# Kernel optimization log

Hardware: AMD Instinct MI355X
Metric: run time of the kernel (lower is better)

## Reference

```python
import jax, jax.numpy as jnp
import numpy as np

N, E, G = 50000, 800000, 16
NODE, HID, OUT, HEADS = 128, 64, 128, 3
NEG_SLOPE = 0.2

def setup_inputs() -> dict:
    key = jax.random.key(0)
    ks = jax.random.split(key, 12)
    h = jax.random.normal(ks[0], (N, NODE), jnp.float32)
    z = jax.random.normal(ks[1], (G, OUT), jnp.float32)
    src = jax.random.randint(ks[2], (E,), 0, N, jnp.int32)
    dst = jax.random.randint(ks[3], (E,), 0, N, jnp.int32)
    graph_id = jnp.sort(jax.random.randint(ks[4], (N,), 0, G, jnp.int32))
    s = 0.1
    fc_w = jax.random.normal(ks[5], (HEADS * HID, NODE), jnp.float32) * s
    attn_l = jax.random.normal(ks[6], (HEADS, HID), jnp.float32) * s
    attn_r = jax.random.normal(ks[7], (HEADS, HID), jnp.float32) * s
    bias = jnp.zeros((HEADS * HID,), jnp.float32)
    lin1_w = jax.random.normal(ks[8], (HID, OUT), jnp.float32) * s
    lin1_b = jnp.zeros((HID,), jnp.float32)
    lin2_w = jax.random.normal(ks[9], (1, 2 * HID), jnp.float32) * s
    lin2_b = jnp.zeros((1,), jnp.float32)
    return dict(h=h, z=z, src=src, dst=dst, graph_id=graph_id, fc_w=fc_w,
                attn_l=attn_l, attn_r=attn_r, bias=bias,
                lin1_w=lin1_w, lin1_b=lin1_b, lin2_w=lin2_w, lin2_b=lin2_b)

def reference(h, z, src, dst, graph_id, fc_w, attn_l, attn_r, bias,
              lin1_w, lin1_b, lin2_w, lin2_b):
    n = h.shape[0]
    # GATConv: projection -> [N, H, D]
    feat = (h @ fc_w.T).reshape(n, HEADS, HID)
    el = jnp.sum(feat * attn_l, axis=-1)  # [N, H]
    er = jnp.sum(feat * attn_r, axis=-1)  # [N, H]
    e = jax.nn.leaky_relu(el[src] + er[dst], NEG_SLOPE)  # [E, H]
    # edge softmax per destination node
    m = jax.ops.segment_max(e, dst, num_segments=n)
    e = jnp.exp(e - m[dst])
    s = jax.ops.segment_sum(e, dst, num_segments=n)
    alpha = e / s[dst]
    # scatter-weighted aggregation
    msg = alpha[:, :, None] * feat[src]  # [E, H, D]
    rst = jax.ops.segment_sum(msg, dst, num_segments=n)  # [N, H, D]
    rst = rst + bias.reshape(HEADS, HID)
    h_d = jnp.mean(rst, axis=1)  # [N, D] (mean over heads)
    # dgl.mean_nodes: per-graph mean pooling
    counts = jax.ops.segment_sum(jnp.ones((n,), h_d.dtype), graph_id, num_segments=G)
    pooled = jax.ops.segment_sum(h_d, graph_id, num_segments=G) / jnp.maximum(counts, 1.0)[:, None]
    z1 = z @ lin1_w.T + lin1_b  # [G, HID]
    cat = jnp.concatenate([pooled, z1], axis=1)  # [G, 2*HID]
    score = jax.nn.sigmoid(cat @ lin2_w.T + lin2_b)  # [G, 1]
    return score
```

## Files before the change

### kernel.cpp

```cpp
#include <hip/hip_runtime.h>
#include <math.h>

#define N_NODES 50000
#define N_EDGES 800000
#define N_GRAPHS 16
#define NODE_F 128
#define HID 64
#define OUT_F 128
#define HEADS 3
#define NEG 0.2f
#define FEAT (HEADS*HID)

typedef float f32x4 __attribute__((ext_vector_type(4)));
typedef float f32x2 __attribute__((ext_vector_type(2)));
typedef short bf16x8 __attribute__((ext_vector_type(8)));

#if defined(__has_builtin)
#if __has_builtin(__builtin_amdgcn_cvt_pk_f32_fp8) && __has_builtin(__builtin_amdgcn_cvt_pk_fp8_f32)
#define USE_FP8 1
#endif
#endif
#ifndef USE_FP8
#define USE_FP8 0
#endif

#if USE_FP8
#define FB 1
#else
#define FB 2
#endif
#define ROWB (FEAT * FB)

#define NBKT ((N_NODES + 63) / 64)
#define H1B 400
#define EPB (N_EDGES / H1B)
#define LROW2 208

__device__ __forceinline__ ushort f2bf(float x) {
  union { float f; unsigned u; } v; v.f = x;
  unsigned r = v.u + 0x7fff + ((v.u >> 16) & 1);
  return (ushort)(r >> 16);
}
__device__ __forceinline__ float bf2f(ushort x) {
  union { unsigned u; float f; } v; v.u = ((unsigned)x) << 16;
  return v.f;
}

__device__ __forceinline__ void feat_store(unsigned char* base, int n, int hh, int dd, float v) {
  size_t off = (size_t)n * ROWB + (hh * HID + dd) * FB;
#if USE_FP8
  base[off] = (unsigned char)(__builtin_amdgcn_cvt_pk_fp8_f32(v, 0.f, 0, false) & 0xff);
#else
  *(ushort*)(base + off) = f2bf(v);
#endif
}

#define ZERO_INTS (N_GRAPHS * HID + N_GRAPHS)
#define ZERO_U4 (ZERO_INTS / 4)
#define ZB ((ZERO_U4 + 255) / 256)
__global__ void kprep(const float* __restrict__ fc_w, ushort* __restrict__ fcb,
                      uint4* __restrict__ zbase) {
  if (blockIdx.x >= 24) {
    int i = (blockIdx.x - 24) * 256 + threadIdx.x;
    if (i < ZERO_U4) zbase[i] = make_uint4(0, 0, 0, 0);
    return;
  }
  int i = blockIdx.x * 256 + threadIdx.x;
  int col = i >> 5;
  int kb = (i & 31) * 4;
  float4 v = *(const float4*)(fc_w + (size_t)col * NODE_F + kb);
  int t = col >> 4, m = col & 15;
  int kk = kb >> 5, kq = (kb >> 3) & 3, j = kb & 7;
  size_t idx0 = ((((size_t)t * 4 + kk) * 4 + kq) * 16 + m) * 8 + j;
  ushort4 o; o.x = f2bf(v.x); o.y = f2bf(v.y); o.z = f2bf(v.z); o.w = f2bf(v.w);
  *(ushort4*)(fcb + idx0) = o;
}

#define GB0 ((N_NODES + 63) / 64)
__global__ __launch_bounds__(256) void k01_fused(
    const float* __restrict__ h, const ushort* __restrict__ fcb,
    const float* __restrict__ attn_l, const float* __restrict__ attn_r,
    const int* __restrict__ dst,
    unsigned char* __restrict__ feat, float* __restrict__ el, float* __restrict__ er,
    int* __restrict__ cnt_g)
{
  __shared__ ushort A[64][136];
  const int tid = threadIdx.x;

  if (blockIdx.x < H1B) {
    int* cnt = (int*)&A[0][0];
    const int blk = blockIdx.x;
    for (int i = tid; i < NBKT; i += 256) cnt[i] = 0;
    __syncthreads();
    const int e0 = blk * EPB;
    for (int i = tid; i < EPB; i += 256)
      atomicAdd(&cnt[dst[e0 + i] >> 6], 1);
    __syncthreads();
    for (int i = tid; i < NBKT; i += 256) cnt_g[(size_t)blk * NBKT + i] = cnt[i];
    return;
  }

  const int n0 = (blockIdx.x - H1B) * 64;
  for (int i = tid; i < 64 * 32; i += 256) {
    int r = i >> 5, c4 = i & 31;
    if (n0 + r < N_NODES) {
      float4 v = *(const float4*)(h + (size_t)(n0 + r) * NODE_F + c4 * 4);
      unsigned lo = f2bf(v.x) | ((unsigned)f2bf(v.y) << 16);
      unsigned hi = f2bf(v.z) | ((unsigned)f2bf(v.w) << 16);
      *(uint2*)&A[r][c4 * 4] = make_uint2(lo, hi);
    }
  }
  __syncthreads();

  const int lane = tid & 63, wv = tid >> 6;
  const int m = lane & 15, kq = lane >> 4;

  f32x4 acc[12];
#pragma unroll
  for (int t = 0; t < 12; t++) acc[t] = (f32x4){0.f, 0.f, 0.f, 0.f};

#pragma unroll
  for (int kk = 0; kk < 4; kk++) {
    bf16x8 af = *(const bf16x8*)&A[wv * 16 + m][kk * 32 + kq * 8];
#pragma unroll
    for (int t = 0; t < 12; t++) {
      const bf16x8 bf = *(const bf16x8*)(fcb + ((((size_t)t * 4 + kk) * 4 + kq) * 16 + m) * 8);
      acc[t] = __builtin_amdgcn_mfma_f32_16x16x32_bf16(af, bf, acc[t], 0, 0, 0);
    }
  }

  const int rbase = n0 + wv * 16 + kq * 4;

#if USE_FP8
  __syncthreads();
  unsigned char* lf = (unsigned char*)&A[0][0];
  const int rloc = wv * 16 + kq * 4;
#pragma unroll
  for (int t = 0; t < 12; t++) {
    const int hh = t >> 2;
    const int dd = (t & 3) * 16 + m;
    const int boff = hh * HID + dd;
#pragma unroll
    for (int reg = 0; reg < 4; reg++) {
      unsigned char q = (unsigned char)(__builtin_amdgcn_cvt_pk_fp8_f32(acc[t][reg], 0.f, 0, false) & 0xff);
      lf[(rloc + reg) * LROW2 + boff] = q;
    }
  }
#else
#pragma unroll
  for (int t = 0; t < 12; t++) {
    const int hh = t >> 2;
    const int dd = (t & 3) * 16 + m;
#pragma unroll
    for (int reg = 0; reg < 4; reg++) {
      int n = rbase + reg;
      if (n < N_NODES) feat_store(feat, n, hh, dd, acc[t][reg]);
    }
  }
#endif

#pragma unroll
  for (int hh = 0; hh < HEADS; hh++) {
    float elv[4] = {0.f, 0.f, 0.f, 0.f};
    float erv[4] = {0.f, 0.f, 0.f, 0.f};
#pragma unroll
    for (int tt = 0; tt < 4; tt++) {
      int t = hh * 4 + tt;
      float al = attn_l[hh * HID + tt * 16 + m];
      float ar = attn_r[hh * HID + tt * 16 + m];
#pragma unroll
      for (int reg = 0; reg < 4; reg++) {
        elv[reg] = fmaf(acc[t][reg], al, elv[reg]);
        erv[reg] = fmaf(acc[t][reg], ar, erv[reg]);
      }
    }
#pragma unroll
    for (int reg = 0; reg < 4; reg++) {
#pragma unroll
      for (int off = 1; off < 16; off <<= 1) {
        elv[reg] += __shfl_xor(elv[reg], off, 64);
        erv[reg] += __shfl_xor(erv[reg], off, 64);
      }
      int n = rbase + reg;
      if (m == 0 && n < N_NODES) {
        el[(size_t)n * 4 + hh] = elv[reg];
        er[(size_t)n * 4 + hh] = erv[reg];
      }
    }
  }

#if USE_FP8
  __syncthreads();
  for (int i = tid; i < 64 * (ROWB / 16); i += 256) {
    int r = i / (ROWB / 16), c = (i % (ROWB / 16)) * 16;
    int n = n0 + r;
    if (n < N_NODES)
      *(uint4*)(feat + (size_t)n * ROWB + c) = *(const uint4*)(lf + r * LROW2 + c);
  }
#endif
}

#define H2A_K 7
__global__ __launch_bounds__(64) void kh2a_scan(
    const int* __restrict__ cnt_g, int* __restrict__ base_bm, int* __restrict__ btot)
{
  const int b = blockIdx.x;
  const int lane = threadIdx.x;
  int v[H2A_K];
  int lt = 0;
#pragma unroll
  for (int j = 0; j < H2A_K; j++) {
    int g = lane * H2A_K + j;
    v[j] = (g < H1B) ? cnt_g[(size_t)g * NBKT + b] : 0;
    lt += v[j];
  }
  int s = lt;
#pragma unroll
  for (int off = 1; off < 64; off <<= 1) {
    int t = __shfl_up(s, off, 64);
    if (lane >= off) s += t;
  }
  int excl = s - lt;
#pragma unroll
  for (int j = 0; j < H2A_K; j++) {
    int g = lane * H2A_K + j;
    if (g < H1B) base_bm[(size_t)b * H1B + g] = excl;
    excl += v[j];
  }
  if (lane == 63) btot[b] = s;
}

__global__ __launch_bounds__(256) void kh3_scatter(
    const int* __restrict__ src, const int* __restrict__ dst,
    const int* __restrict__ btot, const int* __restrict__ base_bm,
    int2* __restrict__ pairs)
{
  __shared__ int cur[NBKT];
  __shared__ int wsum[4];
  const int tid = threadIdx.x, blk = blockIdx.x;
  const int lane = tid & 63, wv = tid >> 6;
  int v[4]; int lt = 0;
#pragma unroll
  for (int j = 0; j < 4; j++) {
    int g = tid * 4 + j;
    v[j] = (g < NBKT) ? btot[g] : 0;
    lt += v[j];
  }
  int s = lt;
#pragma unroll
  for (int off = 1; off < 64; off <<= 1) {
    int t = __shfl_up(s, off, 64);
    if (lane >= off) s += t;
  }
  if (lane == 63) wsum[wv] = s;
  __syncthreads();
  int woff = 0;
#pragma unroll
  for (int w = 0; w < 4; w++) woff += (w < wv) ? wsum[w] : 0;
  int excl = s - lt + woff;
#pragma unroll
  for (int j = 0; j < 4; j++) {
    int g = tid * 4 + j;
    if (g < NBKT) cur[g] = excl + base_bm[(size_t)g * H1B + blk];
    excl += v[j];
  }
  __syncthreads();
  const int e0 = blk * EPB;
  for (int i = tid; i < EPB; i += 256) {
    int e = e0 + i;
    int d = dst[e], sv = src[e];
    int slot = atomicAdd(&cur[d >> 6], 1);
    pairs[slot] = make_int2(sv, d);
  }
}

__global__ __launch_bounds__(256) void kh4_nodesort(
    const int2* __restrict__ pairs, const int* __restrict__ btot,
    int* __restrict__ src_s, int* __restrict__ offs)
{
  __shared__ int nodecnt[64];
  __shared__ int cur[64];
  __shared__ int red_[4];
  __shared__ int lo_s, hi_s;
  const int b = blockIdx.x, tid = threadIdx.x;
  const int lane = tid & 63, wv = tid >> 6;
  int partial = 0;
  for (int i = tid; i < b; i += 256) partial += btot[i];
#pragma unroll
  for (int off = 32; off; off >>= 1) partial += __shfl_xor(partial, off, 64);
  if (lane == 0) red_[wv] = partial;
  if (tid < 64) nodecnt[tid] = 0;
  __syncthreads();
  if (tid == 0) {
    int l = red_[0] + red_[1] + red_[2] + red_[3];
    lo_s = l; hi_s = l + btot[b];
  }
  __syncthreads();
  const int lo = lo_s, hi = hi_s;
  for (int i = lo + tid; i < hi; i += 256)
    atomicAdd(&nodecnt[pairs[i].y & 63], 1);
  __syncthreads();
  if (tid < 64) {
    int v = nodecnt[tid];
    int s = v;
#pragma unroll
    for (int off = 1; off < 64; off <<= 1) {
      int t = __shfl_up(s, off, 64);
      if (tid >= off) s += t;
    }
    int excl = s - v;
    cur[tid] = lo + excl;
    int n = b * 64 + tid;
    if (n < N_NODES) offs[n] = lo + excl;
    if (b == NBKT - 1 && tid == 0) offs[N_NODES] = N_EDGES;
  }
  __syncthreads();
  for (int i = lo + tid; i < hi; i += 256) {
    int2 pr = pairs[i];
    int slot = atomicAdd(&cur[pr.y & 63], 1);
    src_s[slot] = pr.x;
  }
}

__global__ __launch_bounds__(256) void k4_agg(
    const int* __restrict__ offs, const int* __restrict__ src_s,
    const float* __restrict__ el4, const float* __restrict__ er4,
    const unsigned char* __restrict__ feat, const float* __restrict__ bias,
    float* __restrict__ h_d)
{
  __shared__ float4 rec[4][64];
  const int wv = threadIdx.x >> 6, lane = threadIdx.x & 63;
  const int n = blockIdx.x * 4 + wv;
  const int lo = offs[n], hi = offs[n + 1];
  const int half = lane >> 5;
  const int d = lane & 31;
  const char* fb = (const char*)feat;
  const float4 ern = ((const float4*)er4)[n];

  float a0x = 0.f, a0y = 0.f, a1x = 0.f, a1y = 0.f, a2x = 0.f, a2y = 0.f;
  float s0 = 0.f, s1 = 0.f, s2 = 0.f;

  for (int base = lo; base < hi; base += 64) {
    const int cnt = min(64, hi - base);
    if (lane < cnt) {
      int sidx = src_s[base + lane];
      float4 elv = ((const float4*)el4)[sidx];
      float e0 = elv.x + ern.x; e0 = e0 > 0.f ? e0 : NEG * e0;
      float e1 = elv.y + ern.y; e1 = e1 > 0.f ? e1 : NEG * e1;
      float e2 = elv.z + ern.z; e2 = e2 > 0.f ? e2 : NEG * e2;
      float4 c;
      c.x = __expf(e0); c.y = __expf(e1); c.z = __expf(e2);
      c.w = __int_as_float(sidx * ROWB);
      rec[wv][lane] = c;
      s0 += c.x; s1 += c.y; s2 += c.z;
    }
#define K4_BODY(J) do { \
      float4 c = rec[wv][J]; \
      f32x2 f0, f1, f2; \
      if (USE_FP8) { \
        const char* rp = fb + __float_as_int(c.w) + 2 * d; \
        ushort u0 = *(const ushort*)(rp); \
        ushort u1 = *(const ushort*)(rp + HID); \
        ushort u2 = *(const ushort*)(rp + 2 * HID); \
        f0 = __builtin_amdgcn_cvt_pk_f32_fp8(u0, false); \
        f1 = __builtin_amdgcn_cvt_pk_f32_fp8(u1, false); \
        f2 = __builtin_amdgcn_cvt_pk_f32_fp8(u2, false); \
      } else { \
        const char* rp = fb + __float_as_int(c.w) + 4 * d; \
        unsigned q0 = *(const unsigned*)(rp); \
        unsigned q1 = *(const unsigned*)(rp + 2 * HID); \
        unsigned q2 = *(const unsigned*)(rp + 4 * HID); \
        f0.x = bf2f((ushort)(q0 & 0xffff)); f0.y = bf2f((ushort)(q0 >> 16)); \
        f1.x = bf2f((ushort)(q1 & 0xffff)); f1.y = bf2f((ushort)(q1 >> 16)); \
        f2.x = bf2f((ushort)(q2 & 0xffff)); f2.y = bf2f((ushort)(q2 >> 16)); \
      } \
      a0x = fmaf(c.x, f0.x, a0x); a0y = fmaf(c.x, f0.y, a0y); \
      a1x = fmaf(c.y, f1.x, a1x); a1y = fmaf(c.y, f1.y, a1y); \
      a2x = fmaf(c.z, f2.x, a2x); a2y = fmaf(c.z, f2.y, a2y); \
    } while (0)
    int j = half;
    for (; j + 2 < cnt; j += 4) { K4_BODY(j); K4_BODY(j + 2); }
    if (j < cnt) K4_BODY(j);
#undef K4_BODY
  }
  a0x += __shfl_xor(a0x, 32, 64); a0y += __shfl_xor(a0y, 32, 64);
  a1x += __shfl_xor(a1x, 32, 64); a1y += __shfl_xor(a1y, 32, 64);
  a2x += __shfl_xor(a2x, 32, 64); a2y += __shfl_xor(a2y, 32, 64);
#pragma unroll
  for (int off = 32; off; off >>= 1) {
    s0 += __shfl_xor(s0, off, 64);
    s1 += __shfl_xor(s1, off, 64);
    s2 += __shfl_xor(s2, off, 64);
  }
  const float i0 = s0 > 0.f ? 1.f / s0 : 0.f;
  const float i1 = s1 > 0.f ? 1.f / s1 : 0.f;
  const float i2 = s2 > 0.f ? 1.f / s2 : 0.f;
  if (half == 0) {
    float2 b0 = *(const float2*)(bias + 2 * d);
    float2 b1 = *(const float2*)(bias + HID + 2 * d);
    float2 b2 = *(const float2*)(bias + 2 * HID + 2 * d);
    float2 o;
    o.x = (fmaf(a0x, i0, b0.x) + fmaf(a1x, i1, b1.x) + fmaf(a2x, i2, b2.x)) * (1.f / 3.f);
    o.y = (fmaf(a0y, i0, b0.y) + fmaf(a1y, i1, b1.y) + fmaf(a2y, i2, b2.y)) * (1.f / 3.f);
    *(float2*)(h_d + (size_t)n * HID + 2 * d) = o;
  }
}

#define K5_NPB 128
#define K5_NB ((N_NODES + K5_NPB - 1) / K5_NPB)
#define NSEG (K5_NB * 2)
__global__ __launch_bounds__(256) void k5a_partial(
    const int* __restrict__ graph_id, const float* __restrict__ h_d,
    float* __restrict__ pooled_res, int* __restrict__ gcnt_res,
    float* __restrict__ part, int* __restrict__ pg, int* __restrict__ pc)
{
  const int wv = threadIdx.x >> 6, lane = threadIdx.x & 63;
  const int b = blockIdx.x;
  const int n0 = b * K5_NPB;
  const int n1 = min(n0 + K5_NPB, N_NODES);
  const int g_lo = graph_id[n0], g_hi = graph_id[n1 - 1];

  if (g_hi > g_lo + 1) {
    float acc = 0.f; int cur_g = -1; int cnt = 0;
    for (int i = n0 + wv; i < n1; i += 4) {
      int g = graph_id[i];
      if (g != cur_g) {
        if (cur_g >= 0) {
          atomicAdd(&pooled_res[cur_g * HID + lane], acc);
          if (lane == 0) atomicAdd(&gcnt_res[cur_g], cnt);
        }
        acc = 0.f; cnt = 0; cur_g = g;
      }
      acc += h_d[(size_t)i * HID + lane];
      cnt++;
    }
    if (cur_g >= 0) {
      atomicAdd(&pooled_res[cur_g * HID + lane], acc);
      if (lane == 0) atomicAdd(&gcnt_res[cur_g], cnt);
    }
    if (threadIdx.x < 2) pg[b * 2 + threadIdx.x] = -1;
    return;
  }

  float acc_lo = 0.f, acc_hi = 0.f;
  int c_lo = 0, c_hi = 0;
  for (int i = n0 + wv; i < n1; i += 4) {
    int g = graph_id[i];
    float v = h_d[(size_t)i * HID + lane];
    bool hi = (g != g_lo);
    acc_hi += hi ? v : 0.f;
    acc_lo += hi ? 0.f : v;
    c_hi += hi ? 1 : 0;
    c_lo += hi ? 0 : 1;
  }
  __shared__ float ls[2][4][64];
  __shared__ int lc[2][4];
  ls[0][wv][lane] = acc_lo;
  ls[1][wv][lane] = acc_hi;
  if (lane == 0) { lc[0][wv] = c_lo; lc[1][wv] = c_hi; }
  __syncthreads();
  if (wv < 2) {
    float s = ls[wv][0][lane] + ls[wv][1][lane] + ls[wv][2][lane] + ls[wv][3][lane];
    part[((size_t)b * 2 + wv) * HID + lane] = s;
    if (lane == 0) {
      int cnt = lc[wv][0] + lc[wv][1] + lc[wv][2] + lc[wv][3];
      int gg = (wv == 0) ? g_lo : g_hi;
      if (wv == 1 && (g_hi == g_lo || cnt == 0)) gg = -1;
      pg[b * 2 + wv] = gg;
      pc[b * 2 + wv] = cnt;
    }
  }
}

__global__ __launch_bounds__(256) void k6_final(
    const float* __restrict__ part, const int* __restrict__ pg, const int* __restrict__ pc,
    const float* __restrict__ pooled_res, const int* __restrict__ gcnt_res,
    const float* __restrict__ z,
    const float* __restrict__ lin1_w, const float* __restrict__ lin1_b,
    const float* __restrict__ lin2_w, const float* __restrict__ lin2_b,
    float* __restrict__ out)
{
  const int g = blockIdx.x;
  const int tid = threadIdx.x, wv = tid >> 6, lane = tid & 63;
  __shared__ int spg[NSEG], spc[NSEG];
  __shared__ float red[4][HID];
  __shared__ int rc[4];
  __shared__ float cat[2 * HID];

  for (int i = tid; i < NSEG; i += 256) { spg[i] = pg[i]; spc[i] = pc[i]; }
  __syncthreads();

  float acc = 0.f; int cnt = 0;
  for (int s = wv; s < NSEG; s += 4) {
    if (spg[s] == g) {
      acc += part[(size_t)s * HID + lane];
      cnt += spc[s];
    }
  }
  red[wv][lane] = acc;
  if (lane == 0) rc[wv] = cnt;
  __syncthreads();

  if (wv == 0) {
    float s = red[0][lane] + red[1][lane] + red[2][lane] + red[3][lane]
            + pooled_res[g * HID + lane];
    int c = rc[0] + rc[1] + rc[2] + rc[3] + gcnt_res[g];
    cat[lane] = s / (float)(c > 0 ? c : 1);
  }
  if (wv == 1) {
    float s = lin1_b[lane];
    const float* zr = z + g * OUT_F;
    const float* wr = lin1_w + lane * OUT_F;
    for (int k = 0; k < OUT_F; k += 4) {
      float4 zv = *(const float4*)(zr + k);
      float4 wv4 = *(const float4*)(wr + k);
      s = fmaf(zv.x, wv4.x, fmaf(zv.y, wv4.y, fmaf(zv.z, wv4.z, fmaf(zv.w, wv4.w, s))));
    }
    cat[HID + lane] = s;
  }
  __syncthreads();
  if (wv == 0) {
    float s = cat[lane] * lin2_w[lane] + cat[HID + lane] * lin2_w[HID + lane];
#pragma unroll
    for (int off = 32; off; off >>= 1) s += __shfl_xor(s, off, 64);
    if (lane == 0) out[g] = 1.f / (1.f + __expf(-(s + lin2_b[0])));
  }
}

extern "C" void kernel_launch(void* const* d_in, const int* in_sizes, int n_in,
                              void* d_out, int out_size, void* d_ws, size_t ws_size,
                              hipStream_t stream) {
  (void)in_sizes; (void)n_in; (void)out_size; (void)ws_size;
  const float* h      = (const float*)d_in[0];
  const float* z      = (const float*)d_in[1];
  const int*   src    = (const int*)d_in[2];
  const int*   dst    = (const int*)d_in[3];
  const int*   gid    = (const int*)d_in[4];
  const float* fc_w   = (const float*)d_in[5];
  const float* attn_l = (const float*)d_in[6];
  const float* attn_r = (const float*)d_in[7];
  const float* bias   = (const float*)d_in[8];
  const float* lin1_w = (const float*)d_in[9];
  const float* lin1_b = (const float*)d_in[10];
  const float* lin2_w = (const float*)d_in[11];
  const float* lin2_b = (const float*)d_in[12];
  float* out = (float*)d_out;

  int2* pairs       = (int2*)d_ws;
  unsigned char* feat = (unsigned char*)(pairs + N_EDGES);
  float* h_d        = (float*)(feat + (size_t)N_NODES * ROWB);
  float* el         = h_d + (size_t)N_NODES * HID;
  float* er         = el + (size_t)N_NODES * 4;
  float* part       = er + (size_t)N_NODES * 4;
  int* pg           = (int*)(part + (size_t)NSEG * HID);
  int* pc           = pg + NSEG;
  ushort* fcb       = (ushort*)(pc + NSEG);
  float* pooled_res = (float*)(fcb + 192 * NODE_F);
  int* gcnt_res     = (int*)(pooled_res + N_GRAPHS * HID);
  int* offs         = gcnt_res + N_GRAPHS;
  int* src_s        = offs + (N_NODES + 1);
  int* cnt_g        = src_s + N_EDGES;
  int* base_bm      = cnt_g + (size_t)H1B * NBKT;
  int* btot         = base_bm + (size_t)NBKT * H1B;

  kprep<<<24 + ZB, 256, 0, stream>>>(fc_w, fcb, (uint4*)pooled_res);
  k01_fused<<<H1B + GB0, 256, 0, stream>>>(h, fcb, attn_l, attn_r, dst,
                                           feat, el, er, cnt_g);
  kh2a_scan<<<NBKT, 64, 0, stream>>>(cnt_g, base_bm, btot);
  kh3_scatter<<<H1B, 256, 0, stream>>>(src, dst, btot, base_bm, pairs);
  kh4_nodesort<<<NBKT, 256, 0, stream>>>(pairs, btot, src_s, offs);
  k4_agg<<<N_NODES / 4, 256, 0, stream>>>(offs, src_s, el, er, feat, bias, h_d);
  k5a_partial<<<K5_NB, 256, 0, stream>>>(gid, h_d, pooled_res, gcnt_res, part, pg, pc);
  k6_final<<<N_GRAPHS, 256, 0, stream>>>(part, pg, pc, pooled_res, gcnt_res,
                                         z, lin1_w, lin1_b, lin2_w, lin2_b, out);
}
```

Baseline: 202.4 us.

## Merge sort and pooling kernel chains into cooperative kernels with grid sync

Replaces the three-kernel edge bucketing sequence (scan, scatter, node sort) with one cooperative kernel separated by grid-wide syncs. The pooling partial and final scoring kernels are merged the same way. This removes kernel launch gaps and inter-kernel drain between small dependent stages. In exchange it adds grid barrier costs and requires all blocks to be co-resident, with the scatter phase assuming H1B is no larger than NBKT.

```diff
diff --git a/kernel.cpp b/kernel.cpp
--- a/kernel.cpp
+++ b/kernel.cpp
@@ -1,5 +1,8 @@
 #include <hip/hip_runtime.h>
+#include <hip/hip_cooperative_groups.h>
 #include <math.h>
+
+namespace cg = cooperative_groups;
 
 #define N_NODES 50000
 #define N_EDGES 800000
@@ -201,124 +204,124 @@
 }
 
 #define H2A_K 7
-__global__ __launch_bounds__(64) void kh2a_scan(
-    const int* __restrict__ cnt_g, int* __restrict__ base_bm, int* __restrict__ btot)
+__global__ __launch_bounds__(256) void ksort_coop(
+    const int* __restrict__ src, const int* __restrict__ dst,
+    const int* __restrict__ cnt_g, int* __restrict__ base_bm, int* __restrict__ btot,
+    int2* __restrict__ pairs, int* __restrict__ src_s, int* __restrict__ offs)
 {
-  const int b = blockIdx.x;
-  const int lane = threadIdx.x;
-  int v[H2A_K];
-  int lt = 0;
-#pragma unroll
-  for (int j = 0; j < H2A_K; j++) {
-    int g = lane * H2A_K + j;
-    v[j] = (g < H1B) ? cnt_g[(size_t)g * NBKT + b] : 0;
-    lt += v[j];
-  }
-  int s = lt;
-#pragma unroll
-  for (int off = 1; off < 64; off <<= 1) {
-    int t = __shfl_up(s, off, 64);
-    if (lane >= off) s += t;
-  }
-  int excl = s - lt;
-#pragma unroll
-  for (int j = 0; j < H2A_K; j++) {
-    int g = lane * H2A_K + j;
-    if (g < H1B) base_bm[(size_t)b * H1B + g] = excl;
-    excl += v[j];
-  }
-  if (lane == 63) btot[b] = s;
-}
-
-__global__ __launch_bounds__(256) void kh3_scatter(
-    const int* __restrict__ src, const int* __restrict__ dst,
-    const int* __restrict__ btot, const int* __restrict__ base_bm,
-    int2* __restrict__ pairs)
-{
+  cg::grid_group grid = cg::this_grid();
   __shared__ int cur[NBKT];
   __shared__ int wsum[4];
-  const int tid = threadIdx.x, blk = blockIdx.x;
-  const int lane = tid & 63, wv = tid >> 6;
-  int v[4]; int lt = 0;
-#pragma unroll
-  for (int j = 0; j < 4; j++) {
-    int g = tid * 4 + j;
-    v[j] = (g < NBKT) ? btot[g] : 0;
-    lt += v[j];
-  }
-  int s = lt;
-#pragma unroll
-  for (int off = 1; off < 64; off <<= 1) {
-    int t = __shfl_up(s, off, 64);
-    if (lane >= off) s += t;
-  }
-  if (lane == 63) wsum[wv] = s;
-  __syncthreads();
-  int woff = 0;
-#pragma unroll
-  for (int w = 0; w < 4; w++) woff += (w < wv) ? wsum[w] : 0;
-  int excl = s - lt + woff;
-#pragma unroll
-  for (int j = 0; j < 4; j++) {
-    int g = tid * 4 + j;
-    if (g < NBKT) cur[g] = excl + base_bm[(size_t)g * H1B + blk];
-    excl += v[j];
-  }
-  __syncthreads();
-  const int e0 = blk * EPB;
-  for (int i = tid; i < EPB; i += 256) {
-    int e = e0 + i;
-    int d = dst[e], sv = src[e];
-    int slot = atomicAdd(&cur[d >> 6], 1);
-    pairs[slot] = make_int2(sv, d);
-  }
-}
-
-__global__ __launch_bounds__(256) void kh4_nodesort(
-    const int2* __restrict__ pairs, const int* __restrict__ btot,
-    int* __restrict__ src_s, int* __restrict__ offs)
-{
   __shared__ int nodecnt[64];
-  __shared__ int cur[64];
+  __shared__ int cur2[64];
   __shared__ int red_[4];
   __shared__ int lo_s, hi_s;
-  const int b = blockIdx.x, tid = threadIdx.x;
+  const int tid = threadIdx.x;
   const int lane = tid & 63, wv = tid >> 6;
-  int partial = 0;
-  for (int i = tid; i < b; i += 256) partial += btot[i];
-#pragma unroll
-  for (int off = 32; off; off >>= 1) partial += __shfl_xor(partial, off, 64);
-  if (lane == 0) red_[wv] = partial;
-  if (tid < 64) nodecnt[tid] = 0;
-  __syncthreads();
-  if (tid == 0) {
-    int l = red_[0] + red_[1] + red_[2] + red_[3];
-    lo_s = l; hi_s = l + btot[b];
-  }
-  __syncthreads();
-  const int lo = lo_s, hi = hi_s;
-  for (int i = lo + tid; i < hi; i += 256)
-    atomicAdd(&nodecnt[pairs[i].y & 63], 1);
-  __syncthreads();
+
   if (tid < 64) {
-    int v = nodecnt[tid];
-    int s = v;
+    const int b = blockIdx.x;
+    int v[H2A_K];
+    int lt = 0;
+#pragma unroll
+    for (int j = 0; j < H2A_K; j++) {
+      int g = lane * H2A_K + j;
+      v[j] = (g < H1B) ? cnt_g[(size_t)g * NBKT + b] : 0;
+      lt += v[j];
+    }
+    int s = lt;
 #pragma unroll
     for (int off = 1; off < 64; off <<= 1) {
       int t = __shfl_up(s, off, 64);
-      if (tid >= off) s += t;
-    }
-    int excl = s - v;
-    cur[tid] = lo + excl;
-    int n = b * 64 + tid;
-    if (n < N_NODES) offs[n] = lo + excl;
-    if (b == NBKT - 1 && tid == 0) offs[N_NODES] = N_EDGES;
-  }
-  __syncthreads();
-  for (int i = lo + tid; i < hi; i += 256) {
-    int2 pr = pairs[i];
-    int slot = atomicAdd(&cur[pr.y & 63], 1);
-    src_s[slot] = pr.x;
+      if (lane >= off) s += t;
+    }
+    int excl = s - lt;
+#pragma unroll
+    for (int j = 0; j < H2A_K; j++) {
+      int g = lane * H2A_K + j;
+      if (g < H1B) base_bm[(size_t)b * H1B + g] = excl;
+      excl += v[j];
+    }
+    if (lane == 63) btot[b] = s;
+  }
+  grid.sync();
+
+  if (blockIdx.x < H1B) {
+    const int blk = blockIdx.x;
+    int v[4]; int lt = 0;
+#pragma unroll
+    for (int j = 0; j < 4; j++) {
+      int g = tid * 4 + j;
+      v[j] = (g < NBKT) ? btot[g] : 0;
+      lt += v[j];
+    }
+    int s = lt;
+#pragma unroll
+    for (int off = 1; off < 64; off <<= 1) {
+      int t = __shfl_up(s, off, 64);
+      if (lane >= off) s += t;
+    }
+    if (lane == 63) wsum[wv] = s;
+    __syncthreads();
+    int woff = 0;
+#pragma unroll
+    for (int w = 0; w < 4; w++) woff += (w < wv) ? wsum[w] : 0;
+    int excl = s - lt + woff;
+#pragma unroll
+    for (int j = 0; j < 4; j++) {
+      int g = tid * 4 + j;
+      if (g < NBKT) cur[g] = excl + base_bm[(size_t)g * H1B + blk];
+      excl += v[j];
+    }
+    __syncthreads();
+    const int e0 = blk * EPB;
+    for (int i = tid; i < EPB; i += 256) {
+      int e = e0 + i;
+      int d = dst[e], sv = src[e];
+      int slot = atomicAdd(&cur[d >> 6], 1);
+      pairs[slot] = make_int2(sv, d);
+    }
+  }
+  grid.sync();
+
+  {
+    const int b = blockIdx.x;
+    int partial = 0;
+    for (int i = tid; i < b; i += 256) partial += btot[i];
+#pragma unroll
+    for (int off = 32; off; off >>= 1) partial += __shfl_xor(partial, off, 64);
+    if (lane == 0) red_[wv] = partial;
+    if (tid < 64) nodecnt[tid] = 0;
+    __syncthreads();
+    if (tid == 0) {
+      int l = red_[0] + red_[1] + red_[2] + red_[3];
+      lo_s = l; hi_s = l + btot[b];
+    }
+    __syncthreads();
+    const int lo = lo_s, hi = hi_s;
+    for (int i = lo + tid; i < hi; i += 256)
+      atomicAdd(&nodecnt[pairs[i].y & 63], 1);
+    __syncthreads();
+    if (tid < 64) {
+      int v = nodecnt[tid];
+      int s = v;
+#pragma unroll
+      for (int off = 1; off < 64; off <<= 1) {
+        int t = __shfl_up(s, off, 64);
+        if (tid >= off) s += t;
+      }
+      int excl = s - v;
+      cur2[tid] = lo + excl;
+      int n = b * 64 + tid;
+      if (n < N_NODES) offs[n] = lo + excl;
+      if (b == NBKT - 1 && tid == 0) offs[N_NODES] = N_EDGES;
+    }
+    __syncthreads();
+    for (int i = lo + tid; i < hi; i += 256) {
+      int2 pr = pairs[i];
+      int slot = atomicAdd(&cur2[pr.y & 63], 1);
+      src_s[slot] = pr.x;
+    }
   }
 }
 
@@ -409,121 +412,121 @@
 #define K5_NPB 128
 #define K5_NB ((N_NODES + K5_NPB - 1) / K5_NPB)
 #define NSEG (K5_NB * 2)
-__global__ __launch_bounds__(256) void k5a_partial(
+__global__ __launch_bounds__(256) void k56_coop(
     const int* __restrict__ graph_id, const float* __restrict__ h_d,
     float* __restrict__ pooled_res, int* __restrict__ gcnt_res,
-    float* __restrict__ part, int* __restrict__ pg, int* __restrict__ pc)
-{
-  const int wv = threadIdx.x >> 6, lane = threadIdx.x & 63;
-  const int b = blockIdx.x;
-  const int n0 = b * K5_NPB;
-  const int n1 = min(n0 + K5_NPB, N_NODES);
-  const int g_lo = graph_id[n0], g_hi = graph_id[n1 - 1];
-
-  if (g_hi > g_lo + 1) {
-    float acc = 0.f; int cur_g = -1; int cnt = 0;
-    for (int i = n0 + wv; i < n1; i += 4) {
-      int g = graph_id[i];
-      if (g != cur_g) {
-        if (cur_g >= 0) {
-          atomicAdd(&pooled_res[cur_g * HID + lane], acc);
-          if (lane == 0) atomicAdd(&gcnt_res[cur_g], cnt);
-        }
-        acc = 0.f; cnt = 0; cur_g = g;
-      }
-      acc += h_d[(size_t)i * HID + lane];
-      cnt++;
-    }
-    if (cur_g >= 0) {
-      atomicAdd(&pooled_res[cur_g * HID + lane], acc);
-      if (lane == 0) atomicAdd(&gcnt_res[cur_g], cnt);
-    }
-    if (threadIdx.x < 2) pg[b * 2 + threadIdx.x] = -1;
-    return;
-  }
-
-  float acc_lo = 0.f, acc_hi = 0.f;
-  int c_lo = 0, c_hi = 0;
-  for (int i = n0 + wv; i < n1; i += 4) {
-    int g = graph_id[i];
-    float v = h_d[(size_t)i * HID + lane];
-    bool hi = (g != g_lo);
-    acc_hi += hi ? v : 0.f;
-    acc_lo += hi ? 0.f : v;
-    c_hi += hi ? 1 : 0;
-    c_lo += hi ? 0 : 1;
-  }
-  __shared__ float ls[2][4][64];
-  __shared__ int lc[2][4];
-  ls[0][wv][lane] = acc_lo;
-  ls[1][wv][lane] = acc_hi;
-  if (lane == 0) { lc[0][wv] = c_lo; lc[1][wv] = c_hi; }
-  __syncthreads();
-  if (wv < 2) {
-    float s = ls[wv][0][lane] + ls[wv][1][lane] + ls[wv][2][lane] + ls[wv][3][lane];
-    part[((size_t)b * 2 + wv) * HID + lane] = s;
-    if (lane == 0) {
-      int cnt = lc[wv][0] + lc[wv][1] + lc[wv][2] + lc[wv][3];
-      int gg = (wv == 0) ? g_lo : g_hi;
-      if (wv == 1 && (g_hi == g_lo || cnt == 0)) gg = -1;
-      pg[b * 2 + wv] = gg;
-      pc[b * 2 + wv] = cnt;
-    }
-  }
-}
-
-__global__ __launch_bounds__(256) void k6_final(
-    const float* __restrict__ part, const int* __restrict__ pg, const int* __restrict__ pc,
-    const float* __restrict__ pooled_res, const int* __restrict__ gcnt_res,
+    float* __restrict__ part, int* __restrict__ pg, int* __restrict__ pc,
     const float* __restrict__ z,
     const float* __restrict__ lin1_w, const float* __restrict__ lin1_b,
     const float* __restrict__ lin2_w, const float* __restrict__ lin2_b,
     float* __restrict__ out)
 {
-  const int g = blockIdx.x;
-  const int tid = threadIdx.x, wv = tid >> 6, lane = tid & 63;
+  cg::grid_group grid = cg::this_grid();
+  const int tid = threadIdx.x;
+  const int wv = tid >> 6, lane = tid & 63;
+  __shared__ float ls[2][4][64];
+  __shared__ int lc[2][4];
   __shared__ int spg[NSEG], spc[NSEG];
   __shared__ float red[4][HID];
   __shared__ int rc[4];
   __shared__ float cat[2 * HID];
 
-  for (int i = tid; i < NSEG; i += 256) { spg[i] = pg[i]; spc[i] = pc[i]; }
-  __syncthreads();
-
-  float acc = 0.f; int cnt = 0;
-  for (int s = wv; s < NSEG; s += 4) {
-    if (spg[s] == g) {
-      acc += part[(size_t)s * HID + lane];
-      cnt += spc[s];
-    }
-  }
-  red[wv][lane] = acc;
-  if (lane == 0) rc[wv] = cnt;
-  __syncthreads();
-
-  if (wv == 0) {
-    float s = red[0][lane] + red[1][lane] + red[2][lane] + red[3][lane]
-            + pooled_res[g * HID + lane];
-    int c = rc[0] + rc[1] + rc[2] + rc[3] + gcnt_res[g];
-    cat[lane] = s / (float)(c > 0 ? c : 1);
-  }
-  if (wv == 1) {
-    float s = lin1_b[lane];
-    const float* zr = z + g * OUT_F;
-    const float* wr = lin1_w + lane * OUT_F;
-    for (int k = 0; k < OUT_F; k += 4) {
-      float4 zv = *(const float4*)(zr + k);
-      float4 wv4 = *(const float4*)(wr + k);
-      s = fmaf(zv.x, wv4.x, fmaf(zv.y, wv4.y, fmaf(zv.z, wv4.z, fmaf(zv.w, wv4.w, s))));
-    }
-    cat[HID + lane] = s;
-  }
-  __syncthreads();
-  if (wv == 0) {
-    float s = cat[lane] * lin2_w[lane] + cat[HID + lane] * lin2_w[HID + lane];
-#pragma unroll
-    for (int off = 32; off; off >>= 1) s += __shfl_xor(s, off, 64);
-    if (lane == 0) out[g] = 1.f / (1.f + __expf(-(s + lin2_b[0])));
+  {
+    const int b = blockIdx.x;
+    const int n0 = b * K5_NPB;
+    const int n1 = min(n0 + K5_NPB, N_NODES);
+    const int g_lo = graph_id[n0], g_hi = graph_id[n1 - 1];
+
+    if (g_hi > g_lo + 1) {
+      float acc = 0.f; int cur_g = -1; int cnt = 0;
+      for (int i = n0 + wv; i < n1; i += 4) {
+        int g = graph_id[i];
+        if (g != cur_g) {
+          if (cur_g >= 0) {
+            atomicAdd(&pooled_res[cur_g * HID + lane], acc);
+            if (lane == 0) atomicAdd(&gcnt_res[cur_g], cnt);
+          }
+          acc = 0.f; cnt = 0; cur_g = g;
+        }
+        acc += h_d[(size_t)i * HID + lane];
+        cnt++;
+      }
+      if (cur_g >= 0) {
+        atomicAdd(&pooled_res[cur_g * HID + lane], acc);
+        if (lane == 0) atomicAdd(&gcnt_res[cur_g], cnt);
+      }
+      if (tid < 2) pg[b * 2 + tid] = -1;
+    } else {
+      float acc_lo = 0.f, acc_hi = 0.f;
+      int c_lo = 0, c_hi = 0;
+      for (int i = n0 + wv; i < n1; i += 4) {
+        int g = graph_id[i];
+        float v = h_d[(size_t)i * HID + lane];
+        bool hi = (g != g_lo);
+        acc_hi += hi ? v : 0.f;
+        acc_lo += hi ? 0.f : v;
+        c_hi += hi ? 1 : 0;
+        c_lo += hi ? 0 : 1;
+      }
+      ls[0][wv][lane] = acc_lo;
+      ls[1][wv][lane] = acc_hi;
+      if (lane == 0) { lc[0][wv] = c_lo; lc[1][wv] = c_hi; }
+      __syncthreads();
+      if (wv < 2) {
+        float s = ls[wv][0][lane] + ls[wv][1][lane] + ls[wv][2][lane] + ls[wv][3][lane];
+        part[((size_t)b * 2 + wv) * HID + lane] = s;
+        if (lane == 0) {
+          int cnt = lc[wv][0] + lc[wv][1] + lc[wv][2] + lc[wv][3];
+          int gg = (wv == 0) ? g_lo : g_hi;
+          if (wv == 1 && (g_hi == g_lo || cnt == 0)) gg = -1;
+          pg[b * 2 + wv] = gg;
+          pc[b * 2 + wv] = cnt;
+        }
+      }
+    }
+  }
+  grid.sync();
+
+  if (blockIdx.x < N_GRAPHS) {
+    const int g = blockIdx.x;
+    for (int i = tid; i < NSEG; i += 256) { spg[i] = pg[i]; spc[i] = pc[i]; }
+    __syncthreads();
+
+    float acc = 0.f; int cnt = 0;
+    for (int s = wv; s < NSEG; s += 4) {
+      if (spg[s] == g) {
+        acc += part[(size_t)s * HID + lane];
+        cnt += spc[s];
+      }
+    }
+    red[wv][lane] = acc;
+    if (lane == 0) rc[wv] = cnt;
+    __syncthreads();
+
+    if (wv == 0) {
+      float s = red[0][lane] + red[1][lane] + red[2][lane] + red[3][lane]
+              + pooled_res[g * HID + lane];
+      int c = rc[0] + rc[1] + rc[2] + rc[3] + gcnt_res[g];
+      cat[lane] = s / (float)(c > 0 ? c : 1);
+    }
+    if (wv == 1) {
+      float s = lin1_b[lane];
+      const float* zr = z + g * OUT_F;
+      const float* wr = lin1_w + lane * OUT_F;
+      for (int k = 0; k < OUT_F; k += 4) {
+        float4 zv = *(const float4*)(zr + k);
+        float4 wv4 = *(const float4*)(wr + k);
+        s = fmaf(zv.x, wv4.x, fmaf(zv.y, wv4.y, fmaf(zv.z, wv4.z, fmaf(zv.w, wv4.w, s))));
+      }
+      cat[HID + lane] = s;
+    }
+    __syncthreads();
+    if (wv == 0) {
+      float s = cat[lane] * lin2_w[lane] + cat[HID + lane] * lin2_w[HID + lane];
+#pragma unroll
+      for (int off = 32; off; off >>= 1) s += __shfl_xor(s, off, 64);
+      if (lane == 0) out[g] = 1.f / (1.f + __expf(-(s + lin2_b[0])));
+    }
   }
 }
 
@@ -566,11 +569,19 @@
   kprep<<<24 + ZB, 256, 0, stream>>>(fc_w, fcb, (uint4*)pooled_res);
   k01_fused<<<H1B + GB0, 256, 0, stream>>>(h, fcb, attn_l, attn_r, dst,
                                            feat, el, er, cnt_g);
-  kh2a_scan<<<NBKT, 64, 0, stream>>>(cnt_g, base_bm, btot);
-  kh3_scatter<<<H1B, 256, 0, stream>>>(src, dst, btot, base_bm, pairs);
-  kh4_nodesort<<<NBKT, 256, 0, stream>>>(pairs, btot, src_s, offs);
+  {
+    void* args[] = {(void*)&src, (void*)&dst, (void*)&cnt_g, (void*)&base_bm,
+                    (void*)&btot, (void*)&pairs, (void*)&src_s, (void*)&offs};
+    hipLaunchCooperativeKernel((void*)ksort_coop, dim3(NBKT), dim3(256),
+                               args, 0, stream);
+  }
   k4_agg<<<N_NODES / 4, 256, 0, stream>>>(offs, src_s, el, er, feat, bias, h_d);
-  k5a_partial<<<K5_NB, 256, 0, stream>>>(gid, h_d, pooled_res, gcnt_res, part, pg, pc);
-  k6_final<<<N_GRAPHS, 256, 0, stream>>>(part, pg, pc, pooled_res, gcnt_res,
-                                         z, lin1_w, lin1_b, lin2_w, lin2_b, out);
-}
+  {
+    void* args[] = {(void*)&gid, (void*)&h_d, (void*)&pooled_res, (void*)&gcnt_res,
+                    (void*)&part, (void*)&pg, (void*)&pc, (void*)&z,
+                    (void*)&lin1_w, (void*)&lin1_b, (void*)&lin2_w, (void*)&lin2_b,
+                    (void*)&out};
+    hipLaunchCooperativeKernel((void*)k56_coop, dim3(K5_NB), dim3(256),
+                               args, 0, stream);
+  }
+}
```

Result: slower. 449.4 us (+122.1%).
